# Optimization experiments

Hardware: AMD Instinct MI355X
Metric: run time of the kernel (lower is better)

Reference implementation:

```python
import jax, jax.numpy as jnp
import numpy as np

LN_EPS = 1e-5
NEG_SLOPE = 0.01  # torch LeakyReLU default
H, D = 16, 64


def _layernorm(x, g, b):
    m = jnp.mean(x, axis=-1, keepdims=True)
    v = jnp.var(x, axis=-1, keepdims=True)
    return (x - m) * jax.lax.rsqrt(v + LN_EPS) * g + b


def _mlp(x, ln_g, ln_b, W1, b1, W2, b2):
    h = _layernorm(x, ln_g, ln_b)
    h = jax.nn.gelu(h @ W1 + b1, approximate=False)
    return h @ W2 + b2


def _gather_nodes(node_msg, edge_index):
    # node_msg: (b,n,c), edge_index: (b,n,k) -> (b,n,k,c)
    return jax.vmap(lambda nm, ei: nm[ei])(node_msg, edge_index)


def setup_inputs() -> dict:
    key = jax.random.key(0)
    ks = jax.random.split(key, 16)
    b, n, k = 2, 1024, 32
    dim, pdim, msg_dim = 512, 256, 256
    s = 0.02
    inp = {
        'node_repr': jax.random.normal(ks[0], (b, n, dim), jnp.float32),
        'edge_repr': jax.random.normal(ks[1], (b, n, k, pdim), jnp.float32),
        'edge_index': jax.random.randint(ks[2], (b, n, k), 0, n, jnp.int32),
        'edge_mask': jax.random.randint(ks[3], (b, n, k), 0, 2, jnp.int32),
        'mask_bw': jnp.ones((b, n, k, 1), jnp.float32),
        'W_edge_msg': s * jax.random.normal(ks[4], (pdim, msg_dim), jnp.float32),
        'W_node_src': s * jax.random.normal(ks[5], (dim, msg_dim), jnp.float32),
        'W_node_tgt': s * jax.random.normal(ks[6], (dim, msg_dim), jnp.float32),
        'msg_ln_g': jnp.ones((msg_dim,), jnp.float32),
        'msg_ln_b': jnp.zeros((msg_dim,), jnp.float32),
        'msg_W1': s * jax.random.normal(ks[7], (msg_dim, 4 * msg_dim), jnp.float32),
        'msg_b1': jnp.zeros((4 * msg_dim,), jnp.float32),
        'msg_W2': s * jax.random.normal(ks[8], (4 * msg_dim, msg_dim), jnp.float32),
        'msg_b2': jnp.zeros((msg_dim,), jnp.float32),
        'W_gate': jnp.zeros((dim, msg_dim), jnp.float32),   # init_weights: zeros
        'b_gate': -jnp.ones((msg_dim,), jnp.float32),       # init_weights: -1
        'W_out': s * jax.random.normal(ks[9], (msg_dim, dim), jnp.float32),
        'W_msg': s * jax.random.normal(ks[10], (msg_dim, msg_dim), jnp.float32),
        'W_attn_bias': s * jax.random.normal(ks[11], (msg_dim, H), jnp.float32),
        'W_gat_value': s * jax.random.normal(ks[12], (msg_dim, H * D), jnp.float32),
        'W_gat_gate': jnp.zeros((dim, H * D), jnp.float32),
        'b_gat_gate': -jnp.ones((H * D,), jnp.float32),
        'W_gat_out': s * jax.random.normal(ks[13], (H * D, dim), jnp.float32),
        'node_ln_g': jnp.ones((dim,), jnp.float32),
        'node_ln_b': jnp.zeros((dim,), jnp.float32),
        'node_W1': s * jax.random.normal(ks[14], (dim, 4 * dim), jnp.float32),
        'node_b1': jnp.zeros((4 * dim,), jnp.float32),
        'node_W2': s * jax.random.normal(ks[15], (4 * dim, dim), jnp.float32),
        'node_b2': jnp.zeros((dim,), jnp.float32),
    }
    return inp


def reference(node_repr, edge_repr, edge_index, edge_mask, mask_bw,
              W_edge_msg, W_node_src, W_node_tgt,
              msg_ln_g, msg_ln_b, msg_W1, msg_b1, msg_W2, msg_b2,
              W_gate, b_gate, W_out,
              W_msg, W_attn_bias, W_gat_value, W_gat_gate, b_gat_gate, W_gat_out,
              node_ln_g, node_ln_b, node_W1, node_b1, node_W2, node_b2):
    b, n, k = edge_index.shape
    em_bool = edge_mask.astype(bool)          # (b,n,k)
    em_f = edge_mask.astype(node_repr.dtype)

    # edge-wise message: edge proj + gathered src node proj + broadcast tgt node proj
    node_msg = node_repr @ W_node_src                      # (b,n,msg)
    msg = edge_repr @ W_edge_msg \
        + _gather_nodes(node_msg, edge_index) * mask_bw \
        + (node_repr @ W_node_tgt)[:, :, None, :]          # (b,n,k,msg)
    msg = _mlp(msg, msg_ln_g, msg_ln_b, msg_W1, msg_b1, msg_W2, msg_b2)
    msg = jnp.where(em_bool[..., None], msg, 0.0)

    # global (mean-pooled, gated) path
    o = (msg * em_f[..., None]).sum(-2) / (em_f.sum(-1, keepdims=True) + 1e-6)
    o = jax.nn.sigmoid(node_repr @ W_gate + b_gate) * o
    dh = o @ W_out                                         # (b,n,dim)

    # GAT path: per-node attention over its k neighbors
    ab = jnp.where(NEG_SLOPE < 1, jax.nn.leaky_relu(msg @ W_msg, NEG_SLOPE), msg) @ W_attn_bias  # (b,n,k,H)
    ab = jnp.where(em_bool[..., None], ab, -jnp.finfo(ab.dtype).max)
    attn = jax.nn.softmax(ab, axis=2)                      # softmax over k
    v = (msg @ W_gat_value).reshape(b, n, k, H, D)
    og = jnp.einsum('bnkh,bnkhd->bnhd', attn, v).reshape(b, n, H * D)
    og = jax.nn.sigmoid(node_repr @ W_gat_gate + b_gat_gate) * og
    dh = dh + og @ W_gat_out

    # residual + node MLP (dropout is identity in eval mode)
    node_repr = node_repr + dh
    node_repr = node_repr + _mlp(node_repr, node_ln_g, node_ln_b, node_W1, node_b1, node_W2, node_b2)
    return node_repr
```

## Files before the change

kernel.cpp:

```cpp
#include <hip/hip_runtime.h>
#include <hip/hip_bf16.h>

typedef unsigned short u16;
typedef short s16x8 __attribute__((ext_vector_type(8)));
typedef float f32x4 __attribute__((ext_vector_type(4)));
typedef float f32x8 __attribute__((ext_vector_type(8)));
typedef u16 u16x8 __attribute__((ext_vector_type(8)));

#define DEV static __device__ __forceinline__

DEV float b2f(u16 u){ unsigned int i=((unsigned int)u)<<16; float f; __builtin_memcpy(&f,&i,4); return f; }
DEV u16 f2b(float x){ __hip_bfloat16 h=__float2bfloat16(x); u16 u; __builtin_memcpy(&u,&h,2); return u; }
DEV f32x4 MFMA(s16x8 a, s16x8 b, f32x4 c){ return __builtin_amdgcn_mfma_f32_16x16x32_bf16(a,b,c,0,0,0); }
DEV s16x8 LD8(const u16* p){ return *(const s16x8*)p; }
DEV s16x8 cvt8(const float* p){
  s16x8 r;
  #pragma unroll
  for (int i=0;i<8;i++) r[i] = (short)f2b(p[i]);
  return r;
}
DEV float geluf(float x){ return 0.5f*x*(1.0f+erff(x*0.70710678118654752f)); }
DEV float sigmf(float x){ return 1.0f/(1.0f+__expf(-x)); }

DEV void gload16(const u16* g, u16* l){
  __builtin_amdgcn_global_load_lds((const __attribute__((address_space(1))) void*)g,
                                   (__attribute__((address_space(3))) void*)l, 16, 0, 0);
}

DEV s16x8 ldP(const char* b, int row, int sB, int e){
  return *(const s16x8*)(b + row*sB + 2*e);
}
DEV void stP(char* b, int row, int sB, int col, u16 v){
  *(u16*)(b + row*sB + 2*col) = v;
}

#define WS_WeT   0
#define WS_W1T   65536
#define WS_W2T   327680
#define WS_WmT   589824
#define WS_WvT   655360
#define WS_WoT   917504
#define WS_WgoT  1048576
#define WS_nW1T  1572864
#define WS_nW2T  2621440
#define WS_SrcT  3670016
#define WS_TgtT  3801088
#define WS_GateT 3932160
#define WS_GgT   4063232
#define WS_NM    4587520
#define WS_TGT   5111808
#define WS_GP    5636096
#define WS_GG    6160384
#define WS_MSG   8257536
#define WS_U2    8257536
#define WS_X     10354688
#define WS_Y     12451840
#define WS_WM    25034752
#define WS_U1    33423360
#define WS_YE    33947648
#define WS_H     50724864

struct P13 { const float* p[13]; };
__device__ const int TR_START[14] = {0,16,80,144,160,224,256,384,640,896,928,960,992,1120};
__device__ const int TR_R[13]   = {256,256,1024,256,256,256,1024,512,2048,512,512,512,512};
__device__ const int TR_C[13]   = {256,1024,256,256,1024,512,512,2048,512,256,256,256,1024};
__device__ const int TR_DST[13] = {WS_WeT,WS_W1T,WS_W2T,WS_WmT,WS_WvT,WS_WoT,WS_WgoT,
                                   WS_nW1T,WS_nW2T,WS_SrcT,WS_TgtT,WS_GateT,WS_GgT};

__global__ __launch_bounds__(256) void k_transpose(P13 ps, u16* __restrict__ ws){
  __shared__ alignas(16) u16 Ts[64][72];
  const int t = threadIdx.x;
  int bid = blockIdx.x;
  int mi = 0;
  #pragma unroll 1
  while (bid >= TR_START[mi+1]) ++mi;
  const float* src = ps.p[mi];
  const int R = TR_R[mi], C = TR_C[mi];
  u16* dst = ws + TR_DST[mi];
  const int ti = bid - TR_START[mi];
  const int tcn = C >> 6;
  const int tr = ti / tcn, tc = ti % tcn;
  {
    const int row = t >> 2, cs = (t & 3) * 16;
    const float* sp = src + (tr*64 + row)*C + tc*64 + cs;
    u16x8 a, b;
    #pragma unroll
    for (int i=0;i<8;i++){ a[i]=f2b(sp[i]); b[i]=f2b(sp[8+i]); }
    *(u16x8*)&Ts[row][cs]   = a;
    *(u16x8*)&Ts[row][cs+8] = b;
  }
  __syncthreads();
  {
    const int col = t >> 2, rs = (t & 3) * 16;
    u16x8 a, b;
    #pragma unroll
    for (int i=0;i<8;i++){ a[i]=Ts[rs+i][col]; b[i]=Ts[rs+8+i][col]; }
    u16* dp = dst + (tc*64 + col)*R + tr*64 + rs;
    *(u16x8*)dp = a;
    *(u16x8*)(dp+8) = b;
  }
}

__global__ __launch_bounds__(256) void k_proj(const float* __restrict__ node_repr,
                                              const float* __restrict__ bgate,
                                              const float* __restrict__ bgg,
                                              u16* __restrict__ ws){
  const int t=threadIdx.x, lid=t&63, w=t>>6, g=lid>>4, q=lid&15;
  const int rb = blockIdx.x, yb = blockIdx.y;
  const u16* BT; u16* dst; int Nseg, colbase, act=0; const float* bias=nullptr;
  if (yb < 4){ BT=ws+WS_SrcT;  dst=ws+WS_NM; Nseg=256;  colbase=yb*64; }
  else if (yb < 8){ BT=ws+WS_TgtT;  dst=ws+WS_TGT; Nseg=256; colbase=(yb-4)*64; }
  else if (yb < 12){ BT=ws+WS_GateT; dst=ws+WS_GP; Nseg=256; colbase=(yb-8)*64; act=1; bias=bgate; }
  else { BT=ws+WS_GgT; dst=ws+WS_GG; Nseg=1024; colbase=(yb-12)*64; act=1; bias=bgg; }
  const int wr=(w>>1)*32, wcl=(w&1)*32;
  f32x4 acc[2][2] = {};
  for (int kk=0; kk<512; kk+=32){
    s16x8 af[2], bfr[2];
    #pragma unroll
    for (int i=0;i<2;i++) af[i] = cvt8(node_repr + (rb*64 + wr + i*16 + q)*512 + kk + 8*g);
    #pragma unroll
    for (int j=0;j<2;j++) bfr[j] = LD8(BT + (colbase + wcl + j*16 + q)*512 + kk + 8*g);
    #pragma unroll
    for (int i=0;i<2;i++)
      #pragma unroll
      for (int j=0;j<2;j++) acc[i][j] = MFMA(af[i], bfr[j], acc[i][j]);
  }
  #pragma unroll
  for (int i=0;i<2;i++)
    #pragma unroll
    for (int j=0;j<2;j++)
      #pragma unroll
      for (int r=0;r<4;r++){
        const int row = rb*64 + wr + i*16 + g*4 + r;
        const int col = wcl + j*16 + q;
        float v = acc[i][j][r];
        if (act) v = sigmf(v + bias[colbase+col]);
        dst[row*Nseg + colbase + col] = f2b(v);
      }
}

#define GB_S 528
__global__ __launch_bounds__(256) void k_edgepre(
    const float* __restrict__ edge_repr, const int* __restrict__ edge_index,
    const float* __restrict__ mask_bw,
    const float* __restrict__ ln_g, const float* __restrict__ ln_b,
    u16* __restrict__ ws)
{
  __shared__ alignas(16) char Gb[64*GB_S];
  __shared__ alignas(16) u16 As[64*32];
  __shared__ alignas(16) u16 Bs[256*32];
  __shared__ float rsS[4][64], rsQ[4][64];
  __shared__ int idxL[64]; __shared__ float mbwL[64];

  const int t=threadIdx.x, lid=t&63, w=t>>6, g=lid>>4, q=lid&15;
  const int R0 = blockIdx.x * 64;
  const int wc = w * 64;

  if (t < 64){
    idxL[t] = edge_index[R0+t];
    mbwL[t] = mask_bw[R0+t];
  }
  __syncthreads();

  const u16* nm = ws + WS_NM;
  const u16* tg = ws + WS_TGT;

  #pragma unroll
  for (int it=0; it<8; ++it){
    const int v = t + 256*it;
    const int row = v >> 5;
    const int sc  = (v & 31) * 8;
    const int er  = R0 + row;
    const int gnd = er >> 5;
    const int bi  = gnd >> 10;
    const int srow = bi*1024 + idxL[row];
    const float mb = mbwL[row];
    u16x8 nv = *(const u16x8*)(nm + srow*256 + sc);
    u16x8 tv = *(const u16x8*)(tg + gnd*256 + sc);
    u16x8 ov;
    #pragma unroll
    for (int j2=0;j2<8;j2++) ov[j2] = f2b(b2f(nv[j2])*mb + b2f(tv[j2]));
    *(u16x8*)(Gb + row*GB_S + 2*sc) = ov;
  }
  __syncthreads();

  f32x4 acc[4][4];
  #pragma unroll
  for (int i=0;i<4;i++)
    #pragma unroll
    for (int r=0;r<4;r++){
      const int row = i*16 + g*4 + r;
      #pragma unroll
      for (int j=0;j<4;j++){
        const int col = wc + j*16 + q;
        acc[i][j][r] = b2f(*(const u16*)(Gb + row*GB_S + 2*col));
      }
    }
  for (int kk=0; kk<256; kk+=32){
    __syncthreads();
    {
      const int row = t >> 2, c0 = (t & 3) * 8;
      const float* sp = edge_repr + (R0 + row)*256 + kk + c0;
      u16x8 av;
      #pragma unroll
      for (int j2=0;j2<8;j2++) av[j2] = f2b(sp[j2]);
      *(u16x8*)(As + row*32 + c0) = av;
    }
    #pragma unroll
    for (int j=0;j<4;j++){
      const int s = t + 256*j;
      const int brow = s >> 2, ko = (s & 3) * 8;
      u16* ldsB = Bs + (w*64 + 256*j)*8;
      gload16(ws + WS_WeT + brow*256 + kk + ko, ldsB);
    }
    __syncthreads();
    s16x8 af[4], bfr[4];
    #pragma unroll
    for (int i=0;i<4;i++) af[i]  = *(const s16x8*)(As + (i*16+q)*32 + g*8);
    #pragma unroll
    for (int j=0;j<4;j++) bfr[j] = *(const s16x8*)(Bs + (wc + j*16 + q)*32 + g*8);
    #pragma unroll
    for (int i=0;i<4;i++)
      #pragma unroll
      for (int j=0;j<4;j++) acc[i][j] = MFMA(af[i], bfr[j], acc[i][j]);
  }
  #pragma unroll
  for (int i=0;i<4;i++)
    #pragma unroll
    for (int r=0;r<4;r++){
      float s=0.f, s2=0.f;
      #pragma unroll
      for (int j=0;j<4;j++){ float v=acc[i][j][r]; s+=v; s2+=v*v; }
      #pragma unroll
      for (int m=1;m<16;m<<=1){ s += __shfl_xor(s,m,64); s2 += __shfl_xor(s2,m,64); }
      if (q==0){ const int row=i*16+g*4+r; rsS[w][row]=s; rsQ[w][row]=s2; }
    }
  __syncthreads();
  u16* Ye = ws + WS_YE;
  #pragma unroll
  for (int i=0;i<4;i++)
    #pragma unroll
    for (int r=0;r<4;r++){
      const int row=i*16+g*4+r;
      const float s  = rsS[0][row]+rsS[1][row]+rsS[2][row]+rsS[3][row];
      const float s2 = rsQ[0][row]+rsQ[1][row]+rsQ[2][row]+rsQ[3][row];
      const float mean = s*(1.f/256.f);
      const float var  = s2*(1.f/256.f) - mean*mean;
      const float rstd = rsqrtf(var + 1e-5f);
      #pragma unroll
      for (int j=0;j<4;j++){
        const int col = wc + j*16 + q;
        Ye[(R0+row)*256 + col] = f2b((acc[i][j][r]-mean)*rstd*ln_g[col] + ln_b[col]);
      }
    }
}

__global__ __launch_bounds__(256) void k_mlp1(const u16* __restrict__ A,
                                              const u16* __restrict__ BT,
                                              const float* __restrict__ b1,
                                              u16* __restrict__ H){
  __shared__ alignas(16) u16 As[128*32];
  __shared__ alignas(16) u16 Bs[128*32];
  const int t=threadIdx.x, lid=t&63, w=t>>6, g=lid>>4, q=lid&15;
  const int r0 = blockIdx.x*128, n0 = blockIdx.y*128;
  const int wr=(w>>1)*64, wc2=(w&1)*64;
  f32x4 acc[4][4] = {};
  for (int kk=0;kk<256;kk+=32){
    __syncthreads();
    #pragma unroll
    for (int j=0;j<2;j++){
      const int v = t + 256*j;
      const int row = v>>2, sg = (v&3)*8;
      u16* ldsA = As + (w*64 + 256*j)*8;
      u16* ldsB = Bs + (w*64 + 256*j)*8;
      gload16(A  + (r0+row)*256 + kk + sg, ldsA);
      gload16(BT + (n0+row)*256 + kk + sg, ldsB);
    }
    __syncthreads();
    s16x8 af[4], bf_[4];
    #pragma unroll
    for (int i=0;i<4;i++) af[i]  = *(const s16x8*)(As + (wr+i*16+q)*32 + g*8);
    #pragma unroll
    for (int j=0;j<4;j++) bf_[j] = *(const s16x8*)(Bs + (wc2+j*16+q)*32 + g*8);
    #pragma unroll
    for (int i=0;i<4;i++)
      #pragma unroll
      for (int j=0;j<4;j++) acc[i][j] = MFMA(af[i], bf_[j], acc[i][j]);
  }
  #pragma unroll
  for (int i=0;i<4;i++)
    #pragma unroll
    for (int j=0;j<4;j++)
      #pragma unroll
      for (int r=0;r<4;r++){
        const int row = r0 + wr + i*16 + g*4 + r;
        const int col = n0 + wc2 + j*16 + q;
        H[row*1024 + col] = f2b(geluf(acc[i][j][r] + b1[col]));
      }
}

__global__ __launch_bounds__(256) void k_mlp2(const u16* __restrict__ A,
                                              const u16* __restrict__ BT,
                                              const float* __restrict__ b2,
                                              const int* __restrict__ em,
                                              u16* __restrict__ msg){
  __shared__ alignas(16) u16 As[128*32];
  __shared__ alignas(16) u16 Bs[128*32];
  __shared__ int emL[128];
  const int t=threadIdx.x, lid=t&63, w=t>>6, g=lid>>4, q=lid&15;
  const int r0 = blockIdx.x*128, n0 = blockIdx.y*128;
  const int wr=(w>>1)*64, wc2=(w&1)*64;
  if (t < 128) emL[t] = em[r0 + t];
  f32x4 acc[4][4] = {};
  for (int kk=0;kk<1024;kk+=32){
    __syncthreads();
    #pragma unroll
    for (int j=0;j<2;j++){
      const int v = t + 256*j;
      const int row = v>>2, sg = (v&3)*8;
      u16* ldsA = As + (w*64 + 256*j)*8;
      u16* ldsB = Bs + (w*64 + 256*j)*8;
      gload16(A  + (r0+row)*1024 + kk + sg, ldsA);
      gload16(BT + (n0+row)*1024 + kk + sg, ldsB);
    }
    __syncthreads();
    s16x8 af[4], bf_[4];
    #pragma unroll
    for (int i=0;i<4;i++) af[i]  = *(const s16x8*)(As + (wr+i*16+q)*32 + g*8);
    #pragma unroll
    for (int j=0;j<4;j++) bf_[j] = *(const s16x8*)(Bs + (wc2+j*16+q)*32 + g*8);
    #pragma unroll
    for (int i=0;i<4;i++)
      #pragma unroll
      for (int j=0;j<4;j++) acc[i][j] = MFMA(af[i], bf_[j], acc[i][j]);
  }
  #pragma unroll
  for (int i=0;i<4;i++)
    #pragma unroll
    for (int j=0;j<4;j++)
      #pragma unroll
      for (int r=0;r<4;r++){
        const int rl  = wr + i*16 + g*4 + r;
        const int col = n0 + wc2 + j*16 + q;
        float v = acc[i][j][r] + b2[col];
        if (!emL[rl]) v = 0.f;
        msg[(r0+rl)*256 + col] = f2b(v);
      }
}

__global__ __launch_bounds__(256) void k_nmlp1(const u16* __restrict__ A,
                                               const u16* __restrict__ BT,
                                               const float* __restrict__ b1,
                                               u16* __restrict__ H){
  __shared__ alignas(16) u16 As[128*32];
  __shared__ alignas(16) u16 Bs[128*32];
  const int t=threadIdx.x, lid=t&63, w=t>>6, g=lid>>4, q=lid&15;
  const int r0 = blockIdx.x*128, n0 = blockIdx.y*128;
  const int wr=(w>>1)*64, wc2=(w&1)*64;
  f32x4 acc[4][4] = {};
  for (int kk=0;kk<512;kk+=32){
    __syncthreads();
    #pragma unroll
    for (int j=0;j<2;j++){
      const int v = t + 256*j;
      const int row = v>>2, sg = (v&3)*8;
      u16* ldsA = As + (w*64 + 256*j)*8;
      u16* ldsB = Bs + (w*64 + 256*j)*8;
      gload16(A  + (r0+row)*512 + kk + sg, ldsA);
      gload16(BT + (n0+row)*512 + kk + sg, ldsB);
    }
    __syncthreads();
    s16x8 af[4], bf_[4];
    #pragma unroll
    for (int i=0;i<4;i++) af[i]  = *(const s16x8*)(As + (wr+i*16+q)*32 + g*8);
    #pragma unroll
    for (int j=0;j<4;j++) bf_[j] = *(const s16x8*)(Bs + (wc2+j*16+q)*32 + g*8);
    #pragma unroll
    for (int i=0;i<4;i++)
      #pragma unroll
      for (int j=0;j<4;j++) acc[i][j] = MFMA(af[i], bf_[j], acc[i][j]);
  }
  #pragma unroll
  for (int i=0;i<4;i++)
    #pragma unroll
    for (int j=0;j<4;j++)
      #pragma unroll
      for (int r=0;r<4;r++){
        const int row = r0 + wr + i*16 + g*4 + r;
        const int col = n0 + wc2 + j*16 + q;
        H[row*2048 + col] = f2b(geluf(acc[i][j][r] + b1[col]));
      }
}

__global__ __launch_bounds__(256) void k_nmlp2(const u16* __restrict__ A,
                                               const u16* __restrict__ BT,
                                               const float* __restrict__ b2,
                                               const float* __restrict__ Xf,
                                               float* __restrict__ out){
  __shared__ alignas(16) u16 As[64*32];
  __shared__ alignas(16) u16 Bs[64*32];
  const int t=threadIdx.x, lid=t&63, w=t>>6, g=lid>>4, q=lid&15;
  const int r0 = blockIdx.x*64, n0 = blockIdx.y*64;
  const int wr=(w>>1)*32, wc2=(w&1)*32;
  f32x4 acc[2][2] = {};
  for (int kk=0;kk<2048;kk+=32){
    __syncthreads();
    {
      const int row = t>>2, sg = (t&3)*8;
      u16* ldsA = As + (w*64)*8;
      u16* ldsB = Bs + (w*64)*8;
      gload16(A  + (r0+row)*2048 + kk + sg, ldsA);
      gload16(BT + (n0+row)*2048 + kk + sg, ldsB);
    }
    __syncthreads();
    s16x8 af[2], bf_[2];
    #pragma unroll
    for (int i=0;i<2;i++) af[i]  = *(const s16x8*)(As + (wr+i*16+q)*32 + g*8);
    #pragma unroll
    for (int j=0;j<2;j++) bf_[j] = *(const s16x8*)(Bs + (wc2+j*16+q)*32 + g*8);
    #pragma unroll
    for (int i=0;i<2;i++)
      #pragma unroll
      for (int j=0;j<2;j++) acc[i][j] = MFMA(af[i], bf_[j], acc[i][j]);
  }
  #pragma unroll
  for (int i=0;i<2;i++)
    #pragma unroll
    for (int j=0;j<2;j++)
      #pragma unroll
      for (int r=0;r<4;r++){
        const int row = r0 + wr + i*16 + g*4 + r;
        const int col = n0 + wc2 + j*16 + q;
        out[row*512 + col] = acc[i][j][r] + b2[col] + Xf[row*512 + col];
      }
}

#define TM_S 528
#define WB_S 528
#define PB_S 80
#define MB_S 80
__global__ __launch_bounds__(256) void k_attn(const int* __restrict__ edge_mask,
                                              const float* __restrict__ wab,
                                              u16* __restrict__ ws){
  __shared__ alignas(16) char Tmb[32*TM_S];
  __shared__ alignas(16) char Wb[16*WB_S];
  __shared__ alignas(16) char Pb[16*PB_S];
  __shared__ alignas(16) char Mb[256*MB_S];
  __shared__ float Pp[4][32][16];
  __shared__ int emL[32];
  __shared__ float cntS;

  const int t=threadIdx.x, lid=t&63, w=t>>6, g=lid>>4, q=lid&15;
  const int nd = blockIdx.x;
  const int wc = w*64;
  const u16* msg = ws + WS_MSG + nd*32*256;

  if (t < 32) emL[t] = edge_mask[nd*32 + t];
  __syncthreads();
  if (t == 0){ float c=0.f; for (int k=0;k<32;k++) c += emL[k]?1.f:0.f; cntS=c; }

  f32x4 ta[2][4] = {};
  for (int kk=0;kk<256;kk+=32){
    s16x8 af[2], bfr[4];
    #pragma unroll
    for (int i=0;i<2;i++) af[i] = LD8(msg + (i*16+q)*256 + kk + 8*g);
    #pragma unroll
    for (int j=0;j<4;j++) bfr[j] = LD8(ws + WS_WmT + (wc + j*16 + q)*256 + kk + 8*g);
    #pragma unroll
    for (int i=0;i<2;i++)
      #pragma unroll
      for (int j=0;j<4;j++) ta[i][j] = MFMA(af[i], bfr[j], ta[i][j]);
  }
  #pragma unroll
  for (int i=0;i<2;i++)
    #pragma unroll
    for (int j=0;j<4;j++)
      #pragma unroll
      for (int r=0;r<4;r++){
        const int row=i*16+g*4+r, col=wc+j*16+q;
        float v = ta[i][j][r];
        stP(Tmb, row, TM_S, col, f2b(v > 0.f ? v : 0.01f*v));
      }
  {
    #pragma unroll
    for (int h=0;h<16;h++) stP(Wb, h, WB_S, t, f2b(wab[t*16 + h]));
  }
  __syncthreads();
  {
    f32x4 aa[2] = {};
    #pragma unroll
    for (int s2=0;s2<2;s2++){
      const int kk = w*64 + s2*32;
      s16x8 bfr = ldP(Wb, q, WB_S, kk + 8*g);
      #pragma unroll
      for (int i=0;i<2;i++){
        s16x8 af = ldP(Tmb, i*16+q, TM_S, kk + 8*g);
        aa[i] = MFMA(af, bfr, aa[i]);
      }
    }
    #pragma unroll
    for (int i=0;i<2;i++)
      #pragma unroll
      for (int r=0;r<4;r++) Pp[w][i*16+g*4+r][q] = aa[i][r];
  }
  __syncthreads();
  for (int e=t; e<512; e+=256){
    const int k=e>>4, h=e&15;
    float v = Pp[0][k][h]+Pp[1][k][h]+Pp[2][k][h]+Pp[3][k][h];
    Pp[0][k][h] = emL[k] ? v : -3.4028235e38f;
  }
  __syncthreads();
  {
    const int c = t;
    #pragma unroll 1
    for (int k=0;k<32;k++) stP(Mb, c, MB_S, k, msg[k*256 + c]);
  }
  if (t < 16){
    const int h = t;
    float m = -3.4028235e38f;
    for (int k=0;k<32;k++) m = fmaxf(m, Pp[0][k][h]);
    float s = 0.f;
    float ev[32];
    for (int k=0;k<32;k++){ ev[k]=__expf(Pp[0][k][h]-m); s+=ev[k]; }
    const float inv = 1.f/s;
    for (int k=0;k<32;k++) stP(Pb, h, PB_S, k, f2b(ev[k]*inv));
  }
  __syncthreads();
  {
    s16x8 pa = ldP(Pb, q, PB_S, 8*g);
    f32x4 wmac[4] = {};
    #pragma unroll
    for (int j=0;j<4;j++){
      s16x8 mb = ldP(Mb, wc + j*16 + q, MB_S, 8*g);
      wmac[j] = MFMA(pa, mb, wmac[j]);
    }
    u16* wmw = ws + WS_WM;
    #pragma unroll
    for (int j=0;j<4;j++)
      #pragma unroll
      for (int r=0;r<4;r++){
        const int hh = g*4 + r;
        const int col = wc + j*16 + q;
        wmw[hh*(2048*256) + nd*256 + col] = f2b(wmac[j][r]);
      }
  }
  {
    const int c = t;
    float s = 0.f;
    #pragma unroll 1
    for (int k=0;k<32;k++) s += b2f(msg[k*256 + c]);
    const float o = s / (cntS + 1e-6f);
    ws[WS_U1 + nd*256 + c] = f2b(o * b2f(ws[WS_GP + nd*256 + c]));
  }
}

__global__ __launch_bounds__(256) void k_og(u16* __restrict__ ws){
  const int t=threadIdx.x, lid=t&63, w=t>>6, g=lid>>4, q=lid&15;
  const int rb=blockIdx.x, h=blockIdx.y;
  const int wr=(w>>1)*32, wcl=(w&1)*32;
  const u16* A  = ws + WS_WM  + h*(2048*256);
  const u16* BT = ws + WS_WvT;
  f32x4 acc[2][2] = {};
  for (int kk=0;kk<256;kk+=32){
    s16x8 af[2], bfr[2];
    #pragma unroll
    for (int i=0;i<2;i++) af[i] = LD8(A + (rb*64 + wr + i*16 + q)*256 + kk + 8*g);
    #pragma unroll
    for (int j=0;j<2;j++) bfr[j] = LD8(BT + (h*64 + wcl + j*16 + q)*256 + kk + 8*g);
    #pragma unroll
    for (int i=0;i<2;i++)
      #pragma unroll
      for (int j=0;j<2;j++) acc[i][j] = MFMA(af[i], bfr[j], acc[i][j]);
  }
  #pragma unroll
  for (int i=0;i<2;i++)
    #pragma unroll
    for (int j=0;j<2;j++)
      #pragma unroll
      for (int r=0;r<4;r++){
        const int row = rb*64 + wr + i*16 + g*4 + r;
        const int col = h*64 + wcl + j*16 + q;
        const float gv = b2f(ws[WS_GG + row*1024 + col]);
        ws[WS_U2 + row*1024 + col] = f2b(acc[i][j][r] * gv);
      }
}

__global__ __launch_bounds__(256) void k_dh(const float* __restrict__ node_repr, u16* __restrict__ ws){
  const int t=threadIdx.x, lid=t&63, w=t>>6, g=lid>>4, q=lid&15;
  const int rb=blockIdx.x, cb=blockIdx.y*64;
  const int wr=(w>>1)*32, wcl=(w&1)*32;
  float* Xf = (float*)(ws + WS_X);
  f32x4 acc[2][2] = {};
  for (int kk=0;kk<256;kk+=32){
    s16x8 af[2], bfr[2];
    #pragma unroll
    for (int i=0;i<2;i++) af[i] = LD8(ws + WS_U1 + (rb*64 + wr + i*16 + q)*256 + kk + 8*g);
    #pragma unroll
    for (int j=0;j<2;j++) bfr[j] = LD8(ws + WS_WoT + (cb + wcl + j*16 + q)*256 + kk + 8*g);
    #pragma unroll
    for (int i=0;i<2;i++)
      #pragma unroll
      for (int j=0;j<2;j++) acc[i][j] = MFMA(af[i], bfr[j], acc[i][j]);
  }
  for (int kk=0;kk<1024;kk+=32){
    s16x8 af[2], bfr[2];
    #pragma unroll
    for (int i=0;i<2;i++) af[i] = LD8(ws + WS_U2 + (rb*64 + wr + i*16 + q)*1024 + kk + 8*g);
    #pragma unroll
    for (int j=0;j<2;j++) bfr[j] = LD8(ws + WS_WgoT + (cb + wcl + j*16 + q)*1024 + kk + 8*g);
    #pragma unroll
    for (int i=0;i<2;i++)
      #pragma unroll
      for (int j=0;j<2;j++) acc[i][j] = MFMA(af[i], bfr[j], acc[i][j]);
  }
  #pragma unroll
  for (int i=0;i<2;i++)
    #pragma unroll
    for (int j=0;j<2;j++)
      #pragma unroll
      for (int r=0;r<4;r++){
        const int row = rb*64 + wr + i*16 + g*4 + r;
        const int col = cb + wcl + j*16 + q;
        Xf[row*512 + col] = acc[i][j][r] + node_repr[row*512 + col];
      }
}

__global__ __launch_bounds__(256) void k_ln512(const float* __restrict__ g_, const float* __restrict__ b_,
                                               u16* __restrict__ ws){
  const int t=threadIdx.x, wid=t>>6, lane=t&63;
  const int row = blockIdx.x*4 + wid;
  const float* xr = (const float*)(ws + WS_X) + row*512;
  f32x8 xv = *(const f32x8*)(xr + lane*8);
  float s=0.f, s2=0.f;
  #pragma unroll
  for (int i=0;i<8;i++){ s+=xv[i]; s2+=xv[i]*xv[i]; }
  #pragma unroll
  for (int m=1;m<64;m<<=1){ s += __shfl_xor(s,m,64); s2 += __shfl_xor(s2,m,64); }
  const float mean = s*(1.f/512.f);
  const float var  = s2*(1.f/512.f) - mean*mean;
  const float rstd = rsqrtf(var + 1e-5f);
  u16x8 yv;
  #pragma unroll
  for (int i=0;i<8;i++) yv[i] = f2b((xv[i]-mean)*rstd*g_[lane*8+i] + b_[lane*8+i]);
  *(u16x8*)(ws + WS_Y + row*512 + lane*8) = yv;
}

extern "C" void kernel_launch(void* const* d_in, const int* in_sizes, int n_in,
                              void* d_out, int out_size, void* d_ws, size_t ws_size,
                              hipStream_t stream){
  (void)in_sizes; (void)n_in; (void)out_size; (void)ws_size;
  const float* node_repr = (const float*)d_in[0];
  const float* edge_repr = (const float*)d_in[1];
  const int* edge_index = (const int*)d_in[2];
  const int* edge_mask  = (const int*)d_in[3];
  const float* mask_bw = (const float*)d_in[4];
  u16* ws = (u16*)d_ws;

  P13 ps;
  const int srcIdx[13] = {5,10,12,17,19,16,22,25,27,6,7,14,20};
  for (int i=0;i<13;i++) ps.p[i] = (const float*)d_in[srcIdx[i]];

  hipLaunchKernelGGL(k_transpose, dim3(1120), dim3(256), 0, stream, ps, ws);
  hipLaunchKernelGGL(k_proj, dim3(32,28), dim3(256), 0, stream,
                     node_repr, (const float*)d_in[15], (const float*)d_in[21], ws);
  hipLaunchKernelGGL(k_edgepre, dim3(1024), dim3(256), 0, stream,
                     edge_repr, edge_index, mask_bw,
                     (const float*)d_in[8], (const float*)d_in[9], ws);
  for (int grp=0; grp<2; ++grp){
    const u16* Ag = ws + WS_YE + grp*32768*256;
    u16* Hg = ws + WS_H;
    u16* msgg = ws + WS_MSG + grp*32768*256;
    const int* emg = edge_mask + grp*32768;
    hipLaunchKernelGGL(k_mlp1, dim3(256,8), dim3(256), 0, stream,
                       Ag, ws + WS_W1T, (const float*)d_in[11], Hg);
    hipLaunchKernelGGL(k_mlp2, dim3(256,2), dim3(256), 0, stream,
                       Hg, ws + WS_W2T, (const float*)d_in[13], emg, msgg);
  }
  hipLaunchKernelGGL(k_attn, dim3(2048), dim3(256), 0, stream,
                     edge_mask, (const float*)d_in[18], ws);
  hipLaunchKernelGGL(k_og, dim3(32,16), dim3(256), 0, stream, ws);
  hipLaunchKernelGGL(k_dh, dim3(32,8), dim3(256), 0, stream, node_repr, ws);
  hipLaunchKernelGGL(k_ln512, dim3(512), dim3(256), 0, stream,
                     (const float*)d_in[23], (const float*)d_in[24], ws);
  hipLaunchKernelGGL(k_nmlp1, dim3(16,16), dim3(256), 0, stream,
                     ws + WS_Y, ws + WS_nW1T, (const float*)d_in[26], ws + WS_H);
  hipLaunchKernelGGL(k_nmlp2, dim3(32,8), dim3(256), 0, stream,
                     ws + WS_H, ws + WS_nW2T, (const float*)d_in[28],
                     (const float*)(ws + WS_X), (float*)d_out);
}
```

Measured before the change: 388.9 us.

## Split per-node attention kernel into tiled GEMMs plus a lighter softmax kernel

The old per-node attention kernel ran msg@W_msg with direct global loads, refetching W_msg for every node. That step is now a separate 128x128 LDS-tiled GEMM over all 65536 edge rows, followed by its own GEMM for the attention-bias projection, writing fp32 logits to scratch. The remaining per-node kernel only does the masked softmax, the weighted sum of messages and the mean pooling, staging msg in LDS once. The cost is two extra launches and a round trip of the LeakyReLU intermediate through global memory.

Result: faster. 357.4 us (-8.1%).

```diff
diff --git a/kernel.cpp b/kernel.cpp
--- a/kernel.cpp
+++ b/kernel.cpp
@@ -25,13 +25,6 @@
 DEV void gload16(const u16* g, u16* l){
   __builtin_amdgcn_global_load_lds((const __attribute__((address_space(1))) void*)g,
                                    (__attribute__((address_space(3))) void*)l, 16, 0, 0);
-}
-
-DEV s16x8 ldP(const char* b, int row, int sB, int e){
-  return *(const s16x8*)(b + row*sB + 2*e);
-}
-DEV void stP(char* b, int row, int sB, int col, u16 v){
-  *(u16*)(b + row*sB + 2*col) = v;
 }
 
 #define WS_WeT   0
@@ -348,6 +341,260 @@
       }
 }
 
+__global__ __launch_bounds__(256) void k_tm(const u16* __restrict__ A,
+                                            const u16* __restrict__ BT,
+                                            u16* __restrict__ Tm){
+  __shared__ alignas(16) u16 As[128*32];
+  __shared__ alignas(16) u16 Bs[128*32];
+  const int t=threadIdx.x, lid=t&63, w=t>>6, g=lid>>4, q=lid&15;
+  const int r0 = blockIdx.x*128, n0 = blockIdx.y*128;
+  const int wr=(w>>1)*64, wc2=(w&1)*64;
+  f32x4 acc[4][4] = {};
+  for (int kk=0;kk<256;kk+=32){
+    __syncthreads();
+    #pragma unroll
+    for (int j=0;j<2;j++){
+      const int v = t + 256*j;
+      const int row = v>>2, sg = (v&3)*8;
+      u16* ldsA = As + (w*64 + 256*j)*8;
+      u16* ldsB = Bs + (w*64 + 256*j)*8;
+      gload16(A  + (r0+row)*256 + kk + sg, ldsA);
+      gload16(BT + (n0+row)*256 + kk + sg, ldsB);
+    }
+    __syncthreads();
+    s16x8 af[4], bf_[4];
+    #pragma unroll
+    for (int i=0;i<4;i++) af[i]  = *(const s16x8*)(As + (wr+i*16+q)*32 + g*8);
+    #pragma unroll
+    for (int j=0;j<4;j++) bf_[j] = *(const s16x8*)(Bs + (wc2+j*16+q)*32 + g*8);
+    #pragma unroll
+    for (int i=0;i<4;i++)
+      #pragma unroll
+      for (int j=0;j<4;j++) acc[i][j] = MFMA(af[i], bf_[j], acc[i][j]);
+  }
+  #pragma unroll
+  for (int i=0;i<4;i++)
+    #pragma unroll
+    for (int j=0;j<4;j++)
+      #pragma unroll
+      for (int r=0;r<4;r++){
+        const int row = r0 + wr + i*16 + g*4 + r;
+        const int col = n0 + wc2 + j*16 + q;
+        float v = acc[i][j][r];
+        Tm[row*256 + col] = f2b(v > 0.f ? v : 0.01f*v);
+      }
+}
+
+__global__ __launch_bounds__(256) void k_ab(const u16* __restrict__ A,
+                                            const float* __restrict__ Wab,
+                                            float* __restrict__ AB){
+  __shared__ alignas(16) u16 As[128*32];
+  __shared__ alignas(16) char WbT[16*528];
+  const int t=threadIdx.x, lid=t&63, w=t>>6, g=lid>>4, q=lid&15;
+  const int r0 = blockIdx.x*128;
+  {
+    const float* wr_ = Wab + t*16;
+    #pragma unroll
+    for (int h=0;h<16;h++) *(u16*)(WbT + h*528 + 2*t) = f2b(wr_[h]);
+  }
+  f32x4 acc[2] = {};
+  for (int kk=0;kk<256;kk+=32){
+    __syncthreads();
+    #pragma unroll
+    for (int j=0;j<2;j++){
+      const int s = t + 256*j;
+      const int row = s>>2, ko = (s&3)*8;
+      u16* ldsA = As + (w*64 + 256*j)*8;
+      gload16(A + (r0+row)*256 + kk + ko, ldsA);
+    }
+    __syncthreads();
+    s16x8 bf_ = *(const s16x8*)(WbT + q*528 + 2*(kk + 8*g));
+    #pragma unroll
+    for (int i=0;i<2;i++){
+      s16x8 af = *(const s16x8*)(As + (w*32 + i*16 + q)*32 + g*8);
+      acc[i] = MFMA(af, bf_, acc[i]);
+    }
+  }
+  #pragma unroll
+  for (int i=0;i<2;i++)
+    #pragma unroll
+    for (int r=0;r<4;r++){
+      const int row = r0 + w*32 + i*16 + g*4 + r;
+      AB[row*16 + q] = acc[i][r];
+    }
+}
+
+#define AM_S 528
+#define MT_S 80
+__global__ __launch_bounds__(256) void k_attn2(const int* __restrict__ edge_mask,
+                                               u16* __restrict__ ws){
+  __shared__ alignas(16) char Am[32*AM_S];
+  __shared__ alignas(16) char Mt[256*MT_S];
+  __shared__ alignas(16) char Pb[16*80];
+  __shared__ float Pp[32][16];
+  __shared__ int emL[32];
+  __shared__ float cntS;
+
+  const int t=threadIdx.x, lid=t&63, w=t>>6, g=lid>>4, q=lid&15;
+  const int nd = blockIdx.x;
+  const int wc = w*64;
+  const u16* msg = ws + WS_MSG + nd*32*256;
+  const float* ab = (const float*)(ws + WS_YE) + nd*32*16;
+
+  if (t < 32) emL[t] = edge_mask[nd*32 + t];
+  #pragma unroll
+  for (int it=0; it<4; ++it){
+    const int v = t + 256*it;
+    const int row = v >> 5, sc = (v & 31)*8;
+    u16x8 val = *(const u16x8*)(msg + row*256 + sc);
+    *(u16x8*)(Am + row*AM_S + 2*sc) = val;
+  }
+  {
+    const int k = t >> 4, h = t & 15;
+    Pp[k][h]    = ab[k*16 + h];
+    Pp[k+16][h] = ab[(k+16)*16 + h];
+  }
+  __syncthreads();
+  if (t == 0){ float c=0.f; for (int k=0;k<32;k++) c += emL[k]?1.f:0.f; cntS=c; }
+  {
+    const int c = t;
+    #pragma unroll 1
+    for (int k=0;k<32;k++){
+      u16 vv = *(const u16*)(Am + k*AM_S + 2*c);
+      *(u16*)(Mt + c*MT_S + 2*k) = vv;
+    }
+  }
+  if (t < 16){
+    const int h = t;
+    float m = -3.4028235e38f;
+    float pv[32];
+    for (int k=0;k<32;k++){ pv[k] = emL[k] ? Pp[k][h] : -3.4028235e38f; m = fmaxf(m, pv[k]); }
+    float s = 0.f;
+    float ev[32];
+    for (int k=0;k<32;k++){ ev[k]=__expf(pv[k]-m); s+=ev[k]; }
+    const float inv = 1.f/s;
+    for (int k=0;k<32;k++) *(u16*)(Pb + h*80 + 2*k) = f2b(ev[k]*inv);
+  }
+  __syncthreads();
+  {
+    s16x8 pa = *(const s16x8*)(Pb + q*80 + 2*(8*g));
+    f32x4 wmac[4] = {};
+    #pragma unroll
+    for (int j=0;j<4;j++){
+      s16x8 mb = *(const s16x8*)(Mt + (wc + j*16 + q)*MT_S + 2*(8*g));
+      wmac[j] = MFMA(pa, mb, wmac[j]);
+    }
+    u16* wmw = ws + WS_WM;
+    #pragma unroll
+    for (int j=0;j<4;j++)
+      #pragma unroll
+      for (int r=0;r<4;r++){
+        const int hh = g*4 + r;
+        const int col = wc + j*16 + q;
+        wmw[hh*(2048*256) + nd*256 + col] = f2b(wmac[j][r]);
+      }
+  }
+  {
+    const int c = t;
+    float s = 0.f;
+    #pragma unroll 1
+    for (int k=0;k<32;k++) s += b2f(*(const u16*)(Am + k*AM_S + 2*c));
+    const float o = s / (cntS + 1e-6f);
+    ws[WS_U1 + nd*256 + c] = f2b(o * b2f(ws[WS_GP + nd*256 + c]));
+  }
+}
+
+__global__ __launch_bounds__(256) void k_og(u16* __restrict__ ws){
+  const int t=threadIdx.x, lid=t&63, w=t>>6, g=lid>>4, q=lid&15;
+  const int rb=blockIdx.x, h=blockIdx.y;
+  const int wr=(w>>1)*32, wcl=(w&1)*32;
+  const u16* A  = ws + WS_WM  + h*(2048*256);
+  const u16* BT = ws + WS_WvT;
+  f32x4 acc[2][2] = {};
+  for (int kk=0;kk<256;kk+=32){
+    s16x8 af[2], bfr[2];
+    #pragma unroll
+    for (int i=0;i<2;i++) af[i] = LD8(A + (rb*64 + wr + i*16 + q)*256 + kk + 8*g);
+    #pragma unroll
+    for (int j=0;j<2;j++) bfr[j] = LD8(BT + (h*64 + wcl + j*16 + q)*256 + kk + 8*g);
+    #pragma unroll
+    for (int i=0;i<2;i++)
+      #pragma unroll
+      for (int j=0;j<2;j++) acc[i][j] = MFMA(af[i], bfr[j], acc[i][j]);
+  }
+  #pragma unroll
+  for (int i=0;i<2;i++)
+    #pragma unroll
+    for (int j=0;j<2;j++)
+      #pragma unroll
+      for (int r=0;r<4;r++){
+        const int row = rb*64 + wr + i*16 + g*4 + r;
+        const int col = h*64 + wcl + j*16 + q;
+        const float gv = b2f(ws[WS_GG + row*1024 + col]);
+        ws[WS_U2 + row*1024 + col] = f2b(acc[i][j][r] * gv);
+      }
+}
+
+__global__ __launch_bounds__(256) void k_dh(const float* __restrict__ node_repr, u16* __restrict__ ws){
+  const int t=threadIdx.x, lid=t&63, w=t>>6, g=lid>>4, q=lid&15;
+  const int rb=blockIdx.x, cb=blockIdx.y*64;
+  const int wr=(w>>1)*32, wcl=(w&1)*32;
+  float* Xf = (float*)(ws + WS_X);
+  f32x4 acc[2][2] = {};
+  for (int kk=0;kk<256;kk+=32){
+    s16x8 af[2], bfr[2];
+    #pragma unroll
+    for (int i=0;i<2;i++) af[i] = LD8(ws + WS_U1 + (rb*64 + wr + i*16 + q)*256 + kk + 8*g);
+    #pragma unroll
+    for (int j=0;j<2;j++) bfr[j] = LD8(ws + WS_WoT + (cb + wcl + j*16 + q)*256 + kk + 8*g);
+    #pragma unroll
+    for (int i=0;i<2;i++)
+      #pragma unroll
+      for (int j=0;j<2;j++) acc[i][j] = MFMA(af[i], bfr[j], acc[i][j]);
+  }
+  for (int kk=0;kk<1024;kk+=32){
+    s16x8 af[2], bfr[2];
+    #pragma unroll
+    for (int i=0;i<2;i++) af[i] = LD8(ws + WS_U2 + (rb*64 + wr + i*16 + q)*1024 + kk + 8*g);
+    #pragma unroll
+    for (int j=0;j<2;j++) bfr[j] = LD8(ws + WS_WgoT + (cb + wcl + j*16 + q)*1024 + kk + 8*g);
+    #pragma unroll
+    for (int i=0;i<2;i++)
+      #pragma unroll
+      for (int j=0;j<2;j++) acc[i][j] = MFMA(af[i], bfr[j], acc[i][j]);
+  }
+  #pragma unroll
+  for (int i=0;i<2;i++)
+    #pragma unroll
+    for (int j=0;j<2;j++)
+      #pragma unroll
+      for (int r=0;r<4;r++){
+        const int row = rb*64 + wr + i*16 + g*4 + r;
+        const int col = cb + wcl + j*16 + q;
+        Xf[row*512 + col] = acc[i][j][r] + node_repr[row*512 + col];
+      }
+}
+
+__global__ __launch_bounds__(256) void k_ln512(const float* __restrict__ g_, const float* __restrict__ b_,
+                                               u16* __restrict__ ws){
+  const int t=threadIdx.x, wid=t>>6, lane=t&63;
+  const int row = blockIdx.x*4 + wid;
+  const float* xr = (const float*)(ws + WS_X) + row*512;
+  f32x8 xv = *(const f32x8*)(xr + lane*8);
+  float s=0.f, s2=0.f;
+  #pragma unroll
+  for (int i=0;i<8;i++){ s+=xv[i]; s2+=xv[i]*xv[i]; }
+  #pragma unroll
+  for (int m=1;m<64;m<<=1){ s += __shfl_xor(s,m,64); s2 += __shfl_xor(s2,m,64); }
+  const float mean = s*(1.f/512.f);
+  const float var  = s2*(1.f/512.f) - mean*mean;
+  const float rstd = rsqrtf(var + 1e-5f);
+  u16x8 yv;
+  #pragma unroll
+  for (int i=0;i<8;i++) yv[i] = f2b((xv[i]-mean)*rstd*g_[lane*8+i] + b_[lane*8+i]);
+  *(u16x8*)(ws + WS_Y + row*512 + lane*8) = yv;
+}
+
 __global__ __launch_bounds__(256) void k_nmlp1(const u16* __restrict__ A,
                                                const u16* __restrict__ BT,
                                                const float* __restrict__ b1,
@@ -433,216 +680,6 @@
         const int col = n0 + wc2 + j*16 + q;
         out[row*512 + col] = acc[i][j][r] + b2[col] + Xf[row*512 + col];
       }
-}
-
-#define TM_S 528
-#define WB_S 528
-#define PB_S 80
-#define MB_S 80
-__global__ __launch_bounds__(256) void k_attn(const int* __restrict__ edge_mask,
-                                              const float* __restrict__ wab,
-                                              u16* __restrict__ ws){
-  __shared__ alignas(16) char Tmb[32*TM_S];
-  __shared__ alignas(16) char Wb[16*WB_S];
-  __shared__ alignas(16) char Pb[16*PB_S];
-  __shared__ alignas(16) char Mb[256*MB_S];
-  __shared__ float Pp[4][32][16];
-  __shared__ int emL[32];
-  __shared__ float cntS;
-
-  const int t=threadIdx.x, lid=t&63, w=t>>6, g=lid>>4, q=lid&15;
-  const int nd = blockIdx.x;
-  const int wc = w*64;
-  const u16* msg = ws + WS_MSG + nd*32*256;
-
-  if (t < 32) emL[t] = edge_mask[nd*32 + t];
-  __syncthreads();
-  if (t == 0){ float c=0.f; for (int k=0;k<32;k++) c += emL[k]?1.f:0.f; cntS=c; }
-
-  f32x4 ta[2][4] = {};
-  for (int kk=0;kk<256;kk+=32){
-    s16x8 af[2], bfr[4];
-    #pragma unroll
-    for (int i=0;i<2;i++) af[i] = LD8(msg + (i*16+q)*256 + kk + 8*g);
-    #pragma unroll
-    for (int j=0;j<4;j++) bfr[j] = LD8(ws + WS_WmT + (wc + j*16 + q)*256 + kk + 8*g);
-    #pragma unroll
-    for (int i=0;i<2;i++)
-      #pragma unroll
-      for (int j=0;j<4;j++) ta[i][j] = MFMA(af[i], bfr[j], ta[i][j]);
-  }
-  #pragma unroll
-  for (int i=0;i<2;i++)
-    #pragma unroll
-    for (int j=0;j<4;j++)
-      #pragma unroll
-      for (int r=0;r<4;r++){
-        const int row=i*16+g*4+r, col=wc+j*16+q;
-        float v = ta[i][j][r];
-        stP(Tmb, row, TM_S, col, f2b(v > 0.f ? v : 0.01f*v));
-      }
-  {
-    #pragma unroll
-    for (int h=0;h<16;h++) stP(Wb, h, WB_S, t, f2b(wab[t*16 + h]));
-  }
-  __syncthreads();
-  {
-    f32x4 aa[2] = {};
-    #pragma unroll
-    for (int s2=0;s2<2;s2++){
-      const int kk = w*64 + s2*32;
-      s16x8 bfr = ldP(Wb, q, WB_S, kk + 8*g);
-      #pragma unroll
-      for (int i=0;i<2;i++){
-        s16x8 af = ldP(Tmb, i*16+q, TM_S, kk + 8*g);
-        aa[i] = MFMA(af, bfr, aa[i]);
-      }
-    }
-    #pragma unroll
-    for (int i=0;i<2;i++)
-      #pragma unroll
-      for (int r=0;r<4;r++) Pp[w][i*16+g*4+r][q] = aa[i][r];
-  }
-  __syncthreads();
-  for (int e=t; e<512; e+=256){
-    const int k=e>>4, h=e&15;
-    float v = Pp[0][k][h]+Pp[1][k][h]+Pp[2][k][h]+Pp[3][k][h];
-    Pp[0][k][h] = emL[k] ? v : -3.4028235e38f;
-  }
-  __syncthreads();
-  {
-    const int c = t;
-    #pragma unroll 1
-    for (int k=0;k<32;k++) stP(Mb, c, MB_S, k, msg[k*256 + c]);
-  }
-  if (t < 16){
-    const int h = t;
-    float m = -3.4028235e38f;
-    for (int k=0;k<32;k++) m = fmaxf(m, Pp[0][k][h]);
-    float s = 0.f;
-    float ev[32];
-    for (int k=0;k<32;k++){ ev[k]=__expf(Pp[0][k][h]-m); s+=ev[k]; }
-    const float inv = 1.f/s;
-    for (int k=0;k<32;k++) stP(Pb, h, PB_S, k, f2b(ev[k]*inv));
-  }
-  __syncthreads();
-  {
-    s16x8 pa = ldP(Pb, q, PB_S, 8*g);
-    f32x4 wmac[4] = {};
-    #pragma unroll
-    for (int j=0;j<4;j++){
-      s16x8 mb = ldP(Mb, wc + j*16 + q, MB_S, 8*g);
-      wmac[j] = MFMA(pa, mb, wmac[j]);
-    }
-    u16* wmw = ws + WS_WM;
-    #pragma unroll
-    for (int j=0;j<4;j++)
-      #pragma unroll
-      for (int r=0;r<4;r++){
-        const int hh = g*4 + r;
-        const int col = wc + j*16 + q;
-        wmw[hh*(2048*256) + nd*256 + col] = f2b(wmac[j][r]);
-      }
-  }
-  {
-    const int c = t;
-    float s = 0.f;
-    #pragma unroll 1
-    for (int k=0;k<32;k++) s += b2f(msg[k*256 + c]);
-    const float o = s / (cntS + 1e-6f);
-    ws[WS_U1 + nd*256 + c] = f2b(o * b2f(ws[WS_GP + nd*256 + c]));
-  }
-}
-
-__global__ __launch_bounds__(256) void k_og(u16* __restrict__ ws){
-  const int t=threadIdx.x, lid=t&63, w=t>>6, g=lid>>4, q=lid&15;
-  const int rb=blockIdx.x, h=blockIdx.y;
-  const int wr=(w>>1)*32, wcl=(w&1)*32;
-  const u16* A  = ws + WS_WM  + h*(2048*256);
-  const u16* BT = ws + WS_WvT;
-  f32x4 acc[2][2] = {};
-  for (int kk=0;kk<256;kk+=32){
-    s16x8 af[2], bfr[2];
-    #pragma unroll
-    for (int i=0;i<2;i++) af[i] = LD8(A + (rb*64 + wr + i*16 + q)*256 + kk + 8*g);
-    #pragma unroll
-    for (int j=0;j<2;j++) bfr[j] = LD8(BT + (h*64 + wcl + j*16 + q)*256 + kk + 8*g);
-    #pragma unroll
-    for (int i=0;i<2;i++)
-      #pragma unroll
-      for (int j=0;j<2;j++) acc[i][j] = MFMA(af[i], bfr[j], acc[i][j]);
-  }
-  #pragma unroll
-  for (int i=0;i<2;i++)
-    #pragma unroll
-    for (int j=0;j<2;j++)
-      #pragma unroll
-      for (int r=0;r<4;r++){
-        const int row = rb*64 + wr + i*16 + g*4 + r;
-        const int col = h*64 + wcl + j*16 + q;
-        const float gv = b2f(ws[WS_GG + row*1024 + col]);
-        ws[WS_U2 + row*1024 + col] = f2b(acc[i][j][r] * gv);
-      }
-}
-
-__global__ __launch_bounds__(256) void k_dh(const float* __restrict__ node_repr, u16* __restrict__ ws){
-  const int t=threadIdx.x, lid=t&63, w=t>>6, g=lid>>4, q=lid&15;
-  const int rb=blockIdx.x, cb=blockIdx.y*64;
-  const int wr=(w>>1)*32, wcl=(w&1)*32;
-  float* Xf = (float*)(ws + WS_X);
-  f32x4 acc[2][2] = {};
-  for (int kk=0;kk<256;kk+=32){
-    s16x8 af[2], bfr[2];
-    #pragma unroll
-    for (int i=0;i<2;i++) af[i] = LD8(ws + WS_U1 + (rb*64 + wr + i*16 + q)*256 + kk + 8*g);
-    #pragma unroll
-    for (int j=0;j<2;j++) bfr[j] = LD8(ws + WS_WoT + (cb + wcl + j*16 + q)*256 + kk + 8*g);
-    #pragma unroll
-    for (int i=0;i<2;i++)
-      #pragma unroll
-      for (int j=0;j<2;j++) acc[i][j] = MFMA(af[i], bfr[j], acc[i][j]);
-  }
-  for (int kk=0;kk<1024;kk+=32){
-    s16x8 af[2], bfr[2];
-    #pragma unroll
-    for (int i=0;i<2;i++) af[i] = LD8(ws + WS_U2 + (rb*64 + wr + i*16 + q)*1024 + kk + 8*g);
-    #pragma unroll
-    for (int j=0;j<2;j++) bfr[j] = LD8(ws + WS_WgoT + (cb + wcl + j*16 + q)*1024 + kk + 8*g);
-    #pragma unroll
-    for (int i=0;i<2;i++)
-      #pragma unroll
-      for (int j=0;j<2;j++) acc[i][j] = MFMA(af[i], bfr[j], acc[i][j]);
-  }
-  #pragma unroll
-  for (int i=0;i<2;i++)
-    #pragma unroll
-    for (int j=0;j<2;j++)
-      #pragma unroll
-      for (int r=0;r<4;r++){
-        const int row = rb*64 + wr + i*16 + g*4 + r;
-        const int col = cb + wcl + j*16 + q;
-        Xf[row*512 + col] = acc[i][j][r] + node_repr[row*512 + col];
-      }
-}
-
-__global__ __launch_bounds__(256) void k_ln512(const float* __restrict__ g_, const float* __restrict__ b_,
-                                               u16* __restrict__ ws){
-  const int t=threadIdx.x, wid=t>>6, lane=t&63;
-  const int row = blockIdx.x*4 + wid;
-  const float* xr = (const float*)(ws + WS_X) + row*512;
-  f32x8 xv = *(const f32x8*)(xr + lane*8);
-  float s=0.f, s2=0.f;
-  #pragma unroll
-  for (int i=0;i<8;i++){ s+=xv[i]; s2+=xv[i]*xv[i]; }
-  #pragma unroll
-  for (int m=1;m<64;m<<=1){ s += __shfl_xor(s,m,64); s2 += __shfl_xor(s2,m,64); }
-  const float mean = s*(1.f/512.f);
-  const float var  = s2*(1.f/512.f) - mean*mean;
-  const float rstd = rsqrtf(var + 1e-5f);
-  u16x8 yv;
-  #pragma unroll
-  for (int i=0;i<8;i++) yv[i] = f2b((xv[i]-mean)*rstd*g_[lane*8+i] + b_[lane*8+i]);
-  *(u16x8*)(ws + WS_Y + row*512 + lane*8) = yv;
 }
 
 extern "C" void kernel_launch(void* const* d_in, const int* in_sizes, int n_in,
@@ -676,8 +713,12 @@
     hipLaunchKernelGGL(k_mlp2, dim3(256,2), dim3(256), 0, stream,
                        Hg, ws + WS_W2T, (const float*)d_in[13], emg, msgg);
   }
-  hipLaunchKernelGGL(k_attn, dim3(2048), dim3(256), 0, stream,
-                     edge_mask, (const float*)d_in[18], ws);
+  hipLaunchKernelGGL(k_tm, dim3(512,2), dim3(256), 0, stream,
+                     ws + WS_MSG, ws + WS_WmT, ws + WS_H);
+  hipLaunchKernelGGL(k_ab, dim3(512), dim3(256), 0, stream,
+                     ws + WS_H, (const float*)d_in[18], (float*)(ws + WS_YE));
+  hipLaunchKernelGGL(k_attn2, dim3(2048), dim3(256), 0, stream,
+                     edge_mask, ws);
   hipLaunchKernelGGL(k_og, dim3(32,16), dim3(256), 0, stream, ws);
   hipLaunchKernelGGL(k_dh, dim3(32,8), dim3(256), 0, stream, node_repr, ws);
   hipLaunchKernelGGL(k_ln512, dim3(512), dim3(256), 0, stream,
```
